# Performance work log

Measured on AMD Instinct MI355X. Metric: run time of the kernel, lower is better.

Reference implementation:

```python
import jax, jax.numpy as jnp
import numpy as np
import math

B, T, D = 2, 4096, 1024
HD = D // 2                      # head_dim
DEPTH = 12
LAMBDA_INIT = 0.8 - 0.6 * math.exp(-0.3 * DEPTH)
SCALING = HD ** -0.5
EPS = 1e-5


def setup_inputs() -> dict:
    key = jax.random.key(0)
    ks = jax.random.split(key, 11)
    f32 = jnp.float32
    return {
        "q": jax.random.normal(ks[0], (B, T, D), f32),
        "k": jax.random.normal(ks[1], (B, T, D), f32),
        "v": jax.random.normal(ks[2], (B, T, D), f32),
        "Wq": jax.random.normal(ks[3], (D, D), f32) * 0.02,
        "Wk": jax.random.normal(ks[4], (HD, D), f32) * 0.02,
        "Wv": jax.random.normal(ks[5], (D, D), f32) * 0.02,
        "Wo": jax.random.normal(ks[6], (D, D), f32) * 0.02,
        "lambda_q1": jax.random.normal(ks[7], (HD,), f32) * 0.1,
        "lambda_k1": jax.random.normal(ks[8], (HD,), f32) * 0.1,
        "lambda_q2": jax.random.normal(ks[9], (HD,), f32) * 0.1,
        "lambda_k2": jax.random.normal(ks[10], (HD,), f32) * 0.1,
    }


def reference(q, k, v, Wq, Wk, Wv, Wo, lambda_q1, lambda_k1, lambda_q2, lambda_k2):
    b, t, d = q.shape
    s = k.shape[1]
    # projections (Linear with no bias: x @ W.T)
    qp = (q @ Wq.T).reshape(b, t, 2, HD).transpose(0, 2, 1, 3) * SCALING  # [b,2,t,hd]
    kp = k @ Wk.T                                                          # [b,s,hd] (shared by both score heads)
    # dual score maps + softmax over src
    scores = jnp.einsum("bhtd,bsd->bhts", qp, kp)                          # [b,2,t,s]
    scores = jax.nn.softmax(scores.astype(jnp.float32), axis=-1).astype(qp.dtype)
    # lambda-weighted subtraction
    lam1 = jnp.exp(jnp.sum(lambda_q1 * lambda_k1))
    lam2 = jnp.exp(jnp.sum(lambda_q2 * lambda_k2))
    lam = lam1 - lam2 + LAMBDA_INIT
    attn_w = scores[:, 0] - lam * scores[:, 1]                             # [b,t,s]
    # value matmul
    vp = v @ Wv.T                                                          # [b,s,d]
    attn = jnp.einsum("bts,bsd->btd", attn_w, vp)                          # [b,t,d]
    # RMSNorm over last dim (2*head_dim == d), no affine
    rms = jax.lax.rsqrt(jnp.mean(jnp.square(attn), axis=-1, keepdims=True) + EPS)
    attn = attn * rms * (1.0 - LAMBDA_INIT)
    return attn @ Wo.T
```

## Files before the change

kernel.cpp:

```cpp
#include <hip/hip_runtime.h>
#include <stdint.h>
#include <stddef.h>

#define T_   4096
#define BT_  8192
#define SCALING_F      0.04419417382415922f
#define LAMBDA_INIT_F  0.7836057665316212f
#define ONE_MINUS_LI_F 0.2163942334683788f

typedef __attribute__((ext_vector_type(8))) short short8;
typedef __attribute__((ext_vector_type(4))) short short4v;
typedef __attribute__((ext_vector_type(4))) float f32x4;

__device__ __forceinline__ short f2bf(float f){
  uint32_t u = __float_as_uint(f);
  uint32_t r = (u + 0x7fffu + ((u >> 16) & 1u)) >> 16;
  return (short)(uint16_t)r;
}

__device__ __forceinline__ f32x4 mfma16(short8 a, short8 b, f32x4 c){
  return __builtin_amdgcn_mfma_f32_16x16x32_bf16(a, b, c, 0, 0, 0);
}

__device__ __forceinline__ void stage16(short* lds, const short* g){
  __builtin_amdgcn_global_load_lds(
      (const __attribute__((address_space(1))) void*)g,
      (__attribute__((address_space(3))) void*)lds, 16, 0, 0);
}

__global__ void k_cvt(const float* __restrict__ in, short* __restrict__ out, int n4){
  int i  = blockIdx.x*blockDim.x + threadIdx.x;
  int st = gridDim.x*blockDim.x;
  for (; i < n4; i += st){
    float4 v = ((const float4*)in)[i];
    short4v o;
    o.x = f2bf(v.x); o.y = f2bf(v.y); o.z = f2bf(v.z); o.w = f2bf(v.w);
    ((short4v*)out)[i] = o;
  }
}

template<int EPI>
__global__ __launch_bounds__(256, 3) void k_gemm(const short* __restrict__ A,
                                                 const short* __restrict__ Bm,
                                                 void* __restrict__ Cp, int ldc){
  __shared__ short As[128*32];
  __shared__ short Bs[128*32];
  const int tid = threadIdx.x;
  const int w = tid >> 6, l = tid & 63;
  const int m0 = blockIdx.x * 128;
  const int n0 = blockIdx.y * 128;
  const int wr = w >> 1, wc = w & 1;

  f32x4 acc[4][4] = {};

  const short* gA = A  + (size_t)(m0 + w*32 + (l>>2))*1024 + (l&3)*8;
  const short* gB = Bm + (size_t)(n0 + w*32 + (l>>2))*1024 + (l&3)*8;

  for (int k0 = 0; k0 < 1024; k0 += 32){
    stage16(As + w*1024,       gA + k0);
    stage16(As + w*1024 + 512, gA + 16*1024 + k0);
    stage16(Bs + w*1024,       gB + k0);
    stage16(Bs + w*1024 + 512, gB + 16*1024 + k0);
    __syncthreads();
    short8 aF[4], bF[4];
    #pragma unroll
    for (int i = 0; i < 4; i++){
      aF[i] = *(const short8*)&As[(wr*64 + i*16 + (l&15))*32 + (l>>4)*8];
      bF[i] = *(const short8*)&Bs[(wc*64 + i*16 + (l&15))*32 + (l>>4)*8];
    }
    #pragma unroll
    for (int i = 0; i < 4; i++)
      #pragma unroll
      for (int j = 0; j < 4; j++)
        acc[i][j] = mfma16(aF[i], bF[j], acc[i][j]);
    __syncthreads();
  }

  #pragma unroll
  for (int i = 0; i < 4; i++){
    #pragma unroll
    for (int j = 0; j < 4; j++){
      const size_t r0 = (size_t)m0 + wr*64 + i*16 + (l>>4)*4;
      const size_t c  = (size_t)n0 + wc*64 + j*16 + (l&15);
      #pragma unroll
      for (int rg = 0; rg < 4; rg++){
        float v = acc[i][j][rg];
        if (EPI == 2){
          ((float*)Cp)[(r0+rg)*(size_t)ldc + c] = v;
        } else {
          if (EPI == 1) v *= SCALING_F;
          ((short*)Cp)[(r0+rg)*(size_t)ldc + c] = f2bf(v);
        }
      }
    }
  }
}

__global__ __launch_bounds__(512, 2) void k_attn(
    const short* __restrict__ QP, const short* __restrict__ KP,
    const short* __restrict__ VPT,
    const float* __restrict__ lq1, const float* __restrict__ lk1,
    const float* __restrict__ lq2, const float* __restrict__ lk2,
    short* __restrict__ Ab)
{
  __shared__ short Ks[64*512];
  __shared__ short Qs[32*1024];
  __shared__ short Pl[2][32][72];
  __shared__ float lsum[8][16];
  __shared__ float rinv[2][32];
  __shared__ float ssq[8][32];

  int wg = blockIdx.x;
  wg = (wg & 7)*32 + (wg >> 3);
  const int b  = wg >> 7;
  const int t0 = (wg & 127) * 32;

  const int tid = threadIdx.x;
  const int w = tid >> 6, l = tid & 63;

  float s1 = 0.f, s2 = 0.f;
  #pragma unroll
  for (int i = 0; i < 8; i++){
    int idx = l*8 + i;
    s1 += lq1[idx]*lk1[idx];
    s2 += lq2[idx]*lk2[idx];
  }
  #pragma unroll
  for (int off = 1; off < 64; off <<= 1){
    s1 += __shfl_xor(s1, off, 64);
    s2 += __shfl_xor(s2, off, 64);
  }
  const float lam = __expf(s1) - __expf(s2) + LAMBDA_INIT_F;

  const int rc = w >> 1, h = rc >> 1, tch = rc & 1, scb = w & 1;

  f32x4 acc[4][8] = {};
  float lacc[4] = {0.f,0.f,0.f,0.f};

  const short* kpb = KP  + (size_t)(b*T_)*512;
  const short* vbp = VPT + (size_t)(w*128 + (l&15))*BT_ + (size_t)b*T_ + (l>>4)*8;

  const int jx = (l >> 4) ^ (l & 3);
  const int kx = (l >> 2) & 1;

  {
    const short* qsrc = QP + (size_t)(b*T_ + t0)*1024;
    #pragma unroll
    for (int j = 0; j < 4; j++){
      int r = w*4 + j;
      #pragma unroll
      for (int h2 = 0; h2 < 2; h2++)
        stage16(&Qs[r*1024 + h2*512],
                qsrc + (size_t)r*1024 + (h2*64 + (l ^ (r & 7)))*8);
    }
    #pragma unroll
    for (int j = 0; j < 8; j++)
      stage16(&Ks[(w*8 + j)*512], kpb + (size_t)(w*8 + j)*512 + ((l ^ j)*8));
  }
  __syncthreads();

  const short* qp0 = &Qs[(tch*16 + (l&15))*1024 + h*512 + jx*8];
  const short* kp0 = &Ks[(scb*32 + (l&15))*512 + jx*8];
  const short* kp1 = kp0 + 16*512;

  for (int st = 0; st < 64; st++){
    const int s0 = st*64;

    short8 varr[16];
    #pragma unroll
    for (int dc = 0; dc < 8; dc++)
      #pragma unroll
      for (int ks = 0; ks < 2; ks++)
        varr[dc*2 + ks] = *(const short8*)(vbp + (size_t)dc*16*BT_ + s0 + ks*32);
    __builtin_amdgcn_sched_barrier(0);

    f32x4 sa0 = {0.f,0.f,0.f,0.f}, sa1 = {0.f,0.f,0.f,0.f};
    #pragma unroll
    for (int kk = 0; kk < 16; kk++){
      const int ko = ((kk ^ kx) << 5);
      short8 qf = *(const short8*)(qp0 + ko);
      short8 b0 = *(const short8*)(kp0 + ko);
      short8 b1 = *(const short8*)(kp1 + ko);
      sa0 = mfma16(qf, b0, sa0);
      sa1 = mfma16(qf, b1, sa1);
    }

    #pragma unroll
    for (int rg = 0; rg < 4; rg++){
      float e0 = __expf(sa0[rg]);
      float e1 = __expf(sa1[rg]);
      lacc[rg] += e0 + e1;
      int row = tch*16 + (l>>4)*4 + rg;
      Pl[h][row][(2*scb+0)*16 + (l&15)] = f2bf(e0);
      Pl[h][row][(2*scb+1)*16 + (l&15)] = f2bf(e1);
    }

    asm volatile("s_waitcnt lgkmcnt(0)" ::: "memory");
    __builtin_amdgcn_s_barrier();

    if (st + 1 < 64){
      const short* ksrc = kpb + (size_t)((st+1)*64 + w*8)*512;
      #pragma unroll
      for (int j = 0; j < 8; j++)
        stage16(&Ks[(w*8 + j)*512], ksrc + (size_t)j*512 + ((l ^ j)*8));
    }

    #pragma unroll
    for (int ks = 0; ks < 2; ks++){
      short8 pa[4];
      #pragma unroll
      for (int rc2 = 0; rc2 < 4; rc2++)
        pa[rc2] = *(const short8*)&Pl[rc2>>1][(rc2&1)*16 + (l&15)][ks*32 + (l>>4)*8];
      #pragma unroll
      for (int dc = 0; dc < 8; dc++)
        #pragma unroll
        for (int rc2 = 0; rc2 < 4; rc2++)
          acc[rc2][dc] = mfma16(pa[rc2], varr[dc*2 + ks], acc[rc2][dc]);
    }

    __syncthreads();
  }

  #pragma unroll
  for (int off = 1; off < 16; off <<= 1)
    #pragma unroll
    for (int rg = 0; rg < 4; rg++) lacc[rg] += __shfl_xor(lacc[rg], off, 16);
  if ((l & 15) == 0){
    #pragma unroll
    for (int rg = 0; rg < 4; rg++) lsum[w][(l>>4)*4 + rg] = lacc[rg];
  }
  __syncthreads();
  if (tid < 64){
    int hh = tid >> 5, t = tid & 31;
    int rcc = hh*2 + (t >> 4), ric = t & 15;
    rinv[hh][t] = 1.0f / (lsum[rcc*2][ric] + lsum[rcc*2+1][ric]);
  }
  __syncthreads();

  float ps[2][4] = {};
  #pragma unroll
  for (int tc = 0; tc < 2; tc++){
    #pragma unroll
    for (int dc = 0; dc < 8; dc++){
      #pragma unroll
      for (int rg = 0; rg < 4; rg++){
        int t32 = tc*16 + (l>>4)*4 + rg;
        float o = acc[tc][dc][rg]*rinv[0][t32] - lam*acc[2+tc][dc][rg]*rinv[1][t32];
        ps[tc][rg] += o*o;
      }
    }
  }
  #pragma unroll
  for (int tc = 0; tc < 2; tc++)
    #pragma unroll
    for (int off = 1; off < 16; off <<= 1)
      #pragma unroll
      for (int rg = 0; rg < 4; rg++) ps[tc][rg] += __shfl_xor(ps[tc][rg], off, 16);
  if ((l & 15) == 0){
    #pragma unroll
    for (int tc = 0; tc < 2; tc++)
      #pragma unroll
      for (int rg = 0; rg < 4; rg++) ssq[w][tc*16 + (l>>4)*4 + rg] = ps[tc][rg];
  }
  __syncthreads();

  #pragma unroll
  for (int tc = 0; tc < 2; tc++){
    #pragma unroll
    for (int rg = 0; rg < 4; rg++){
      int t32 = tc*16 + (l>>4)*4 + rg;
      float tot = 0.f;
      #pragma unroll
      for (int w8 = 0; w8 < 8; w8++) tot += ssq[w8][t32];
      float scale = rsqrtf(tot*(1.0f/1024.0f) + 1e-5f) * ONE_MINUS_LI_F;
      short* orow = Ab + (size_t)(b*T_ + t0 + t32)*1024 + w*128 + (l&15);
      #pragma unroll
      for (int dc = 0; dc < 8; dc++){
        float o = acc[tc][dc][rg]*rinv[0][t32] - lam*acc[2+tc][dc][rg]*rinv[1][t32];
        orow[dc*16] = f2bf(o*scale);
      }
    }
  }
}

extern "C" void kernel_launch(void* const* d_in, const int* in_sizes, int n_in,
                              void* d_out, int out_size, void* d_ws, size_t ws_size,
                              hipStream_t stream){
  const float* q   = (const float*)d_in[0];
  const float* k   = (const float*)d_in[1];
  const float* v   = (const float*)d_in[2];
  const float* Wq  = (const float*)d_in[3];
  const float* Wk  = (const float*)d_in[4];
  const float* Wv  = (const float*)d_in[5];
  const float* Wo  = (const float*)d_in[6];
  const float* lq1 = (const float*)d_in[7];
  const float* lk1 = (const float*)d_in[8];
  const float* lq2 = (const float*)d_in[9];
  const float* lk2 = (const float*)d_in[10];

  short* ws   = (short*)d_ws;
  short* qb   = ws;
  short* kb   = qb  + (size_t)8192*1024;
  short* vb   = kb  + (size_t)8192*1024;
  short* Wqb  = vb  + (size_t)8192*1024;
  short* Wkb  = Wqb + (size_t)1024*1024;
  short* Wvb  = Wkb + (size_t)512*1024;
  short* Wob  = Wvb + (size_t)1024*1024;
  short* QPb  = Wob + (size_t)1024*1024;
  short* KPb  = QPb + (size_t)8192*1024;
  short* VPTb = KPb + (size_t)8192*512;
  short* Ab   = qb;

  auto cvt = [&](const float* in, short* out, size_t n){
    int n4 = (int)(n/4);
    int grid = (n4 + 255)/256; if (grid > 2048) grid = 2048;
    k_cvt<<<grid, 256, 0, stream>>>(in, out, n4);
  };
  cvt(q,  qb,  (size_t)8192*1024);
  cvt(k,  kb,  (size_t)8192*1024);
  cvt(v,  vb,  (size_t)8192*1024);
  cvt(Wq, Wqb, (size_t)1024*1024);
  cvt(Wk, Wkb, (size_t)512*1024);
  cvt(Wv, Wvb, (size_t)1024*1024);
  cvt(Wo, Wob, (size_t)1024*1024);

  k_gemm<1><<<dim3(64, 8), 256, 0, stream>>>(qb, Wqb, QPb, 1024);
  k_gemm<0><<<dim3(64, 4), 256, 0, stream>>>(kb, Wkb, KPb, 512);
  k_gemm<0><<<dim3(8, 64), 256, 0, stream>>>(Wvb, vb, VPTb, 8192);
  k_attn<<<dim3(256), 512, 0, stream>>>(QPb, KPb, VPTb, lq1, lk1, lq2, lk2, Ab);
  k_gemm<2><<<dim3(64, 8), 256, 0, stream>>>(Ab, Wob, d_out, 1024);
}
```

Before: 452.5 us.

## Split attention work across 16 waves per block and raise MFMA priority

The attention kernel now launches 1024 threads per block instead of 512. Each wave handles a 16-column key slice for scores and a 64-wide slice of the value output, so per-wave accumulators and V registers are halved. Staging loops, the LDS reduction arrays and the output indexing are adjusted to match. s_setprio is also placed around the MFMA loops. The aim is more latency hiding within a block and lower register pressure. In exchange each wave issues smaller MFMA chains, there are more barrier participants, and only one block fits per CU.

```diff
diff --git a/kernel.cpp b/kernel.cpp
--- a/kernel.cpp
+++ b/kernel.cpp
@@ -96,7 +96,7 @@
   }
 }
 
-__global__ __launch_bounds__(512, 2) void k_attn(
+__global__ __launch_bounds__(1024) void k_attn(
     const short* __restrict__ QP, const short* __restrict__ KP,
     const short* __restrict__ VPT,
     const float* __restrict__ lq1, const float* __restrict__ lk1,
@@ -106,9 +106,9 @@
   __shared__ short Ks[64*512];
   __shared__ short Qs[32*1024];
   __shared__ short Pl[2][32][72];
-  __shared__ float lsum[8][16];
+  __shared__ float lsum[16][16];
   __shared__ float rinv[2][32];
-  __shared__ float ssq[8][32];
+  __shared__ float ssq[16][32];
 
   int wg = blockIdx.x;
   wg = (wg & 7)*32 + (wg >> 3);
@@ -132,13 +132,13 @@
   }
   const float lam = __expf(s1) - __expf(s2) + LAMBDA_INIT_F;
 
-  const int rc = w >> 1, h = rc >> 1, tch = rc & 1, scb = w & 1;
-
-  f32x4 acc[4][8] = {};
+  const int rc = w >> 2, h = rc >> 1, tch = rc & 1, scb = w & 3;
+
+  f32x4 acc[4][4] = {};
   float lacc[4] = {0.f,0.f,0.f,0.f};
 
   const short* kpb = KP  + (size_t)(b*T_)*512;
-  const short* vbp = VPT + (size_t)(w*128 + (l&15))*BT_ + (size_t)b*T_ + (l>>4)*8;
+  const short* vbp = VPT + (size_t)(w*64 + (l&15))*BT_ + (size_t)b*T_ + (l>>4)*8;
 
   const int jx = (l >> 4) ^ (l & 3);
   const int kx = (l >> 2) & 1;
@@ -146,63 +146,64 @@
   {
     const short* qsrc = QP + (size_t)(b*T_ + t0)*1024;
     #pragma unroll
-    for (int j = 0; j < 4; j++){
-      int r = w*4 + j;
+    for (int j = 0; j < 2; j++){
+      int r = w*2 + j;
       #pragma unroll
       for (int h2 = 0; h2 < 2; h2++)
         stage16(&Qs[r*1024 + h2*512],
                 qsrc + (size_t)r*1024 + (h2*64 + (l ^ (r & 7)))*8);
     }
     #pragma unroll
-    for (int j = 0; j < 8; j++)
-      stage16(&Ks[(w*8 + j)*512], kpb + (size_t)(w*8 + j)*512 + ((l ^ j)*8));
+    for (int j = 0; j < 4; j++){
+      int r = w*4 + j;
+      stage16(&Ks[r*512], kpb + (size_t)r*512 + ((l ^ (r & 7))*8));
+    }
   }
   __syncthreads();
 
   const short* qp0 = &Qs[(tch*16 + (l&15))*1024 + h*512 + jx*8];
-  const short* kp0 = &Ks[(scb*32 + (l&15))*512 + jx*8];
-  const short* kp1 = kp0 + 16*512;
+  const short* kp0 = &Ks[(scb*16 + (l&15))*512 + jx*8];
 
   for (int st = 0; st < 64; st++){
     const int s0 = st*64;
 
-    short8 varr[16];
-    #pragma unroll
-    for (int dc = 0; dc < 8; dc++)
+    short8 varr[8];
+    #pragma unroll
+    for (int dc = 0; dc < 4; dc++)
       #pragma unroll
       for (int ks = 0; ks < 2; ks++)
         varr[dc*2 + ks] = *(const short8*)(vbp + (size_t)dc*16*BT_ + s0 + ks*32);
     __builtin_amdgcn_sched_barrier(0);
 
-    f32x4 sa0 = {0.f,0.f,0.f,0.f}, sa1 = {0.f,0.f,0.f,0.f};
+    f32x4 sa0 = {0.f,0.f,0.f,0.f};
+    __builtin_amdgcn_s_setprio(1);
     #pragma unroll
     for (int kk = 0; kk < 16; kk++){
       const int ko = ((kk ^ kx) << 5);
       short8 qf = *(const short8*)(qp0 + ko);
       short8 b0 = *(const short8*)(kp0 + ko);
-      short8 b1 = *(const short8*)(kp1 + ko);
       sa0 = mfma16(qf, b0, sa0);
-      sa1 = mfma16(qf, b1, sa1);
-    }
+    }
+    __builtin_amdgcn_s_setprio(0);
 
     #pragma unroll
     for (int rg = 0; rg < 4; rg++){
       float e0 = __expf(sa0[rg]);
-      float e1 = __expf(sa1[rg]);
-      lacc[rg] += e0 + e1;
+      lacc[rg] += e0;
       int row = tch*16 + (l>>4)*4 + rg;
-      Pl[h][row][(2*scb+0)*16 + (l&15)] = f2bf(e0);
-      Pl[h][row][(2*scb+1)*16 + (l&15)] = f2bf(e1);
+      Pl[h][row][scb*16 + (l&15)] = f2bf(e0);
     }
 
     asm volatile("s_waitcnt lgkmcnt(0)" ::: "memory");
     __builtin_amdgcn_s_barrier();
 
     if (st + 1 < 64){
-      const short* ksrc = kpb + (size_t)((st+1)*64 + w*8)*512;
-      #pragma unroll
-      for (int j = 0; j < 8; j++)
-        stage16(&Ks[(w*8 + j)*512], ksrc + (size_t)j*512 + ((l ^ j)*8));
+      const short* ksrc = kpb + (size_t)((st+1)*64)*512;
+      #pragma unroll
+      for (int j = 0; j < 4; j++){
+        int r = w*4 + j;
+        stage16(&Ks[r*512], ksrc + (size_t)r*512 + ((l ^ (r & 7))*8));
+      }
     }
 
     #pragma unroll
@@ -211,11 +212,13 @@
       #pragma unroll
       for (int rc2 = 0; rc2 < 4; rc2++)
         pa[rc2] = *(const short8*)&Pl[rc2>>1][(rc2&1)*16 + (l&15)][ks*32 + (l>>4)*8];
-      #pragma unroll
-      for (int dc = 0; dc < 8; dc++)
+      __builtin_amdgcn_s_setprio(1);
+      #pragma unroll
+      for (int dc = 0; dc < 4; dc++)
         #pragma unroll
         for (int rc2 = 0; rc2 < 4; rc2++)
           acc[rc2][dc] = mfma16(pa[rc2], varr[dc*2 + ks], acc[rc2][dc]);
+      __builtin_amdgcn_s_setprio(0);
     }
 
     __syncthreads();
@@ -233,7 +236,8 @@
   if (tid < 64){
     int hh = tid >> 5, t = tid & 31;
     int rcc = hh*2 + (t >> 4), ric = t & 15;
-    rinv[hh][t] = 1.0f / (lsum[rcc*2][ric] + lsum[rcc*2+1][ric]);
+    rinv[hh][t] = 1.0f / (lsum[rcc*4+0][ric] + lsum[rcc*4+1][ric] +
+                          lsum[rcc*4+2][ric] + lsum[rcc*4+3][ric]);
   }
   __syncthreads();
 
@@ -241,7 +245,7 @@
   #pragma unroll
   for (int tc = 0; tc < 2; tc++){
     #pragma unroll
-    for (int dc = 0; dc < 8; dc++){
+    for (int dc = 0; dc < 4; dc++){
       #pragma unroll
       for (int rg = 0; rg < 4; rg++){
         int t32 = tc*16 + (l>>4)*4 + rg;
@@ -271,11 +275,11 @@
       int t32 = tc*16 + (l>>4)*4 + rg;
       float tot = 0.f;
       #pragma unroll
-      for (int w8 = 0; w8 < 8; w8++) tot += ssq[w8][t32];
+      for (int w16 = 0; w16 < 16; w16++) tot += ssq[w16][t32];
       float scale = rsqrtf(tot*(1.0f/1024.0f) + 1e-5f) * ONE_MINUS_LI_F;
-      short* orow = Ab + (size_t)(b*T_ + t0 + t32)*1024 + w*128 + (l&15);
-      #pragma unroll
-      for (int dc = 0; dc < 8; dc++){
+      short* orow = Ab + (size_t)(b*T_ + t0 + t32)*1024 + w*64 + (l&15);
+      #pragma unroll
+      for (int dc = 0; dc < 4; dc++){
         float o = acc[tc][dc][rg]*rinv[0][t32] - lam*acc[2+tc][dc][rg]*rinv[1][t32];
         orow[dc*16] = f2bf(o*scale);
       }
@@ -327,6 +331,6 @@
   k_gemm<1><<<dim3(64, 8), 256, 0, stream>>>(qb, Wqb, QPb, 1024);
   k_gemm<0><<<dim3(64, 4), 256, 0, stream>>>(kb, Wkb, KPb, 512);
   k_gemm<0><<<dim3(8, 64), 256, 0, stream>>>(Wvb, vb, VPTb, 8192);
-  k_attn<<<dim3(256), 512, 0, stream>>>(QPb, KPb, VPTb, lq1, lk1, lq2, lk2, Ab);
+  k_attn<<<dim3(256), 1024, 0, stream>>>(QPb, KPb, VPTb, lq1, lk1, lq2, lk2, Ab);
   k_gemm<2><<<dim3(64, 8), 256, 0, stream>>>(Ab, Wob, d_out, 1024);
 }
```

Result: slower. 585.6 us (+29.4%).
